# Kernel optimization log

Measured on AMD Instinct MI355X. Metric: run time of the kernel, lower is better.

## Reference

```python
import jax, jax.numpy as jnp
import numpy as np

NUM_HEADS = 12
DROP = 0.5


def setup_inputs() -> dict:
    key = jax.random.key(0)
    k1, k2, k3, k4 = jax.random.split(key, 4)
    B, N, C = 64, 577, 768
    x = jax.random.normal(k1, (B, N, C), dtype=jnp.float32)
    mask = jax.random.uniform(k2, (B, NUM_HEADS, N - 1), dtype=jnp.float32)
    Wqkv = jax.random.normal(k3, (C, 3 * C), dtype=jnp.float32) * 0.02
    bqkv = jnp.zeros((3 * C,), dtype=jnp.float32)
    Wproj = jax.random.normal(k4, (C, C), dtype=jnp.float32) * 0.02
    bproj = jnp.zeros((C,), dtype=jnp.float32)
    return {"x": x, "mask": mask, "Wqkv": Wqkv, "bqkv": bqkv,
            "Wproj": Wproj, "bproj": bproj}


def _drop_tokens(t, idx):
    # t: [B,H,N,D]; keep CLS token, gather sorted random indices from the rest
    rest = jnp.take_along_axis(t[:, :, 1:, :], idx[..., None], axis=2)
    return jnp.concatenate([t[:, :, :1, :], rest], axis=2)


def reference(x, mask, Wqkv, bqkv, Wproj, bproj):
    B, N, C = x.shape
    H = NUM_HEADS
    D = C // H
    scale = D ** -0.5
    target_len = N - int(N * DROP)  # kept tokens incl. CLS

    qkv = (x @ Wqkv + bqkv).reshape(B, N, 3, H, D)
    qkv = jnp.transpose(qkv, (2, 0, 3, 1, 4))  # [3,B,H,N,D]
    q, k, v = qkv[0], qkv[1], qkv[2]

    # random token drop (rand branch): topk of random mask, sort indices
    _, idx = jax.lax.top_k(mask, target_len - 1)  # [B,H,target_len-1]
    idx = jnp.sort(idx, axis=-1)
    k_p = _drop_tokens(k, idx)  # [B,H,target_len,D]
    v_p = _drop_tokens(v, idx)

    attn = jax.nn.softmax(
        jnp.einsum('bhnd,bhmd->bhnm', q, k_p) * scale, axis=-1)
    out = jnp.einsum('bhnm,bhmd->bhnd', attn, v_p)
    out = jnp.transpose(out, (0, 2, 1, 3)).reshape(B, N, C)
    return out @ Wproj + bproj
```

## Files before the change

### kernel.cpp

```cpp
#include <hip/hip_runtime.h>
#include <stdint.h>

#define B_      64
#define N_TOK   577
#define C_      768
#define H_      12
#define BH_     768
#define M_ROWS  36928
#define M_PAD   36992
#define KEEP    289
#define KP      320

typedef __attribute__((ext_vector_type(8))) short   bf16x8;
typedef __attribute__((ext_vector_type(4))) float   floatx4;
typedef __attribute__((ext_vector_type(4))) short   short4v;

static __device__ __forceinline__ unsigned short f2bf(float f) {
  union { float f; unsigned u; } a; a.f = f;
  unsigned u = a.u;
  u = u + 0x7FFFu + ((u >> 16) & 1u);
  return (unsigned short)(u >> 16);
}

static __device__ __forceinline__ void gl_lds16(const void* g, void* l) {
  __builtin_amdgcn_global_load_lds(
      (const __attribute__((address_space(1))) void*)g,
      (__attribute__((address_space(3))) void*)l, 16, 0, 0);
}

__global__ void topk_kernel(const float* __restrict__ mask, int* __restrict__ pos) {
  __shared__ float vals[576];
  __shared__ int woff[9];
  int row = blockIdx.x;
  int t = threadIdx.x;
  float v = mask[(size_t)row * 576 + t];
  vals[t] = v;
  __syncthreads();
  int rank = 0;
  for (int j = 0; j < 576; ++j) {
    float u = vals[j];
    rank += ((u > v) || (u == v && j < t)) ? 1 : 0;
  }
  bool sel = rank < (KEEP - 1);
  unsigned long long ball = __ballot(sel ? 1 : 0);
  int lane = t & 63, w = t >> 6;
  int lp = __popcll(ball & ((1ull << lane) - 1ull));
  if (lane == 0) woff[w] = __popcll(ball);
  __syncthreads();
  int base = 0;
  for (int i = 0; i < w; ++i) base += woff[i];
  pos[(size_t)row * 577 + 1 + t] = sel ? (1 + base + lp) : -1;
  if (t == 0) pos[(size_t)row * 577] = 0;
}

__global__ void convx_kernel(const float* __restrict__ x, unsigned short* __restrict__ xb) {
  size_t i = ((size_t)blockIdx.x * 256 + threadIdx.x) * 4;
  short4v o;
  if (i < (size_t)M_ROWS * C_) {
    float4 v = *(const float4*)(x + i);
    o.x = (short)f2bf(v.x); o.y = (short)f2bf(v.y);
    o.z = (short)f2bf(v.z); o.w = (short)f2bf(v.w);
  } else {
    o.x = 0; o.y = 0; o.z = 0; o.w = 0;
  }
  *(short4v*)(xb + i) = o;
}

__global__ void convwT_kernel(const float* __restrict__ W, unsigned short* __restrict__ Wt,
                              int N) {
  __shared__ unsigned short tile[64 * 72];
  int n0 = blockIdx.x * 64, k0 = blockIdx.y * 64;
  int t = threadIdx.x;
  for (int p = 0; p < 4; ++p) {
    int s = p * 256 + t;
    int k = s >> 4, nc = s & 15;
    float4 v = *(const float4*)(W + (size_t)(k0 + k) * N + n0 + nc * 4);
    short4v o;
    o.x = (short)f2bf(v.x); o.y = (short)f2bf(v.y);
    o.z = (short)f2bf(v.z); o.w = (short)f2bf(v.w);
    *(short4v*)(tile + k * 72 + nc * 4) = o;
  }
  __syncthreads();
  for (int p = 0; p < 2; ++p) {
    int s = p * 256 + t;
    int n = s >> 3, kc = s & 7;
    bf16x8 o;
    for (int j = 0; j < 8; ++j) o[j] = (short)tile[(kc * 8 + j) * 72 + n];
    *(bf16x8*)(Wt + (size_t)(n0 + n) * 768 + k0 + kc * 8) = o;
  }
}

__global__ void zeropad_kernel(unsigned short* __restrict__ Kp, unsigned short* __restrict__ Vp) {
  size_t idx = (size_t)blockIdx.x * 256 + threadIdx.x;
  int bh = (int)(idx / (31 * 64));
  int rem = (int)(idx % (31 * 64));
  int r = KEEP + rem / 64, d = rem & 63;
  size_t o = ((size_t)bh * KP + r) * 64 + d;
  Kp[o] = 0; Vp[o] = 0;
}

static __device__ __forceinline__ void stage_half512(const unsigned short* src,
                                                     unsigned short* lds, int tid) {
#pragma unroll
  for (int c = 0; c < 2; ++c) {
    int s = c * 512 + tid;
    int r = s >> 3, cs = s & 7;
    int gc = (cs ^ (r & 7)) << 3;
    gl_lds16(src + (size_t)r * 768 + gc, lds + s * 8);
  }
}

static __device__ __forceinline__ void gemm256_core(
    const unsigned short* __restrict__ A, const unsigned short* __restrict__ Bt,
    int m0, int n0, int tid, unsigned short* As, unsigned short* Bs,
    floatx4 (&acc)[8][4]) {
  const int lane = tid & 63, wv = tid >> 6;
  const int quad = lane >> 4, lcol = lane & 15;
  const int wm = wv >> 2, wn = wv & 3;
  const int swz = lcol & 7;

#define STG_A(kt, half) stage_half512(A  + (size_t)(m0 + 128*(half)) * 768 + (kt)*64, \
                                      As + ((kt)&1)*16384 + (half)*8192, tid)
#define STG_B(kt, half) stage_half512(Bt + (size_t)(n0 + 128*(half)) * 768 + (kt)*64, \
                                      Bs + ((kt)&1)*16384 + (half)*8192, tid)

  STG_A(0, 0); STG_A(0, 1); STG_B(0, 0); STG_B(0, 1);
  STG_A(1, 0); STG_A(1, 1); STG_B(1, 0);
  asm volatile("s_waitcnt vmcnt(6)" ::: "memory");
  __builtin_amdgcn_s_barrier();

  for (int t = 0; t < 12; ++t) {
    const unsigned short* Asl = As + (t & 1) * 16384;
    const unsigned short* Bsl = Bs + (t & 1) * 16384;

    bf16x8 af[8][2], bfr[4][2];
#pragma unroll
    for (int ks = 0; ks < 2; ++ks) {
      int cc = ks * 4 + quad;
      int co = (cc ^ swz) << 3;
#pragma unroll
      for (int i = 0; i < 8; ++i)
        af[i][ks]  = *(const bf16x8*)(Asl + (wm * 128 + i * 16 + lcol) * 64 + co);
#pragma unroll
      for (int j = 0; j < 4; ++j)
        bfr[j][ks] = *(const bf16x8*)(Bsl + (wn * 64 + j * 16 + lcol) * 64 + co);
    }
    if (t + 1 < 12) STG_B(t + 1, 1);
    asm volatile("s_waitcnt lgkmcnt(0)" ::: "memory");
    __builtin_amdgcn_sched_barrier(0);
    __builtin_amdgcn_s_barrier();
    __builtin_amdgcn_s_setprio(1);
#pragma unroll
    for (int i = 0; i < 2; ++i)
#pragma unroll
      for (int j = 0; j < 4; ++j)
#pragma unroll
        for (int ks = 0; ks < 2; ++ks)
          acc[i][j] = __builtin_amdgcn_mfma_f32_16x16x32_bf16(af[i][ks], bfr[j][ks], acc[i][j], 0, 0, 0);
    __builtin_amdgcn_s_setprio(0);
    __builtin_amdgcn_s_barrier();

#pragma unroll
    for (int p = 1; p < 4; ++p) {
      if (t + 2 < 12) {
        if (p == 1)      STG_A(t + 2, 0);
        else if (p == 2) STG_A(t + 2, 1);
        else             STG_B(t + 2, 0);
      }
      __builtin_amdgcn_s_barrier();
      __builtin_amdgcn_s_setprio(1);
#pragma unroll
      for (int i = 2 * p; i < 2 * p + 2; ++i)
#pragma unroll
        for (int j = 0; j < 4; ++j)
#pragma unroll
          for (int ks = 0; ks < 2; ++ks)
            acc[i][j] = __builtin_amdgcn_mfma_f32_16x16x32_bf16(af[i][ks], bfr[j][ks], acc[i][j], 0, 0, 0);
      __builtin_amdgcn_s_setprio(0);
      if (p == 3) {
        if (t < 10)       asm volatile("s_waitcnt vmcnt(6)" ::: "memory");
        else if (t == 10) asm volatile("s_waitcnt vmcnt(0)" ::: "memory");
      }
      __builtin_amdgcn_s_barrier();
    }
  }
#undef STG_A
#undef STG_B
}

__global__ __launch_bounds__(512) void qkv_gemm_kernel(
    const unsigned short* __restrict__ A, const unsigned short* __restrict__ Bt,
    const float* __restrict__ bias, const int* __restrict__ pos,
    unsigned short* __restrict__ Q, unsigned short* __restrict__ Kp,
    unsigned short* __restrict__ Vp) {
  __shared__ unsigned short As[2 * 16384];
  __shared__ unsigned short Bs[2 * 16384];
  const int tid = threadIdx.x;
  const int lane = tid & 63, wv = tid >> 6;
  const int quad = lane >> 4, lcol = lane & 15;
  const int wm = wv >> 2, wn = wv & 3;
  int orig = blockIdx.x;
  int xcd = orig & 7, loc = orig >> 3;
  int wgid = (xcd < 1 ? xcd * 164 : 164 + (xcd - 1) * 163) + loc;
  const int m_t = wgid / 9, n_t = wgid % 9;
  const int m0 = m_t * 256, n0 = n_t * 256;

  floatx4 acc[8][4] = {};
  gemm256_core(A, Bt, m0, n0, tid, As, Bs, acc);

  const int nbase = n0 + wn * 64;
  const int which = nbase / 768;
  const int h = (nbase - which * 768) >> 6;
  float bv[4];
#pragma unroll
  for (int nt = 0; nt < 4; ++nt) bv[nt] = bias[nbase + nt * 16 + lcol];
#pragma unroll
  for (int i = 0; i < 8; ++i) {
#pragma unroll
    for (int r = 0; r < 4; ++r) {
      int m = m0 + wm * 128 + i * 16 + quad * 4 + r;
      if (m >= M_ROWS) continue;
      int b = m / 577, t = m - b * 577;
      int bh = b * 12 + h;
      if (which == 0) {
        size_t base = ((size_t)bh * 577 + t) * 64;
#pragma unroll
        for (int nt = 0; nt < 4; ++nt)
          Q[base + nt * 16 + lcol] = f2bf(acc[i][nt][r] + bv[nt]);
      } else {
        int p = pos[(size_t)bh * 577 + t];
        if (p >= 0) {
          size_t base = ((size_t)bh * KP + p) * 64;
          if (which == 1) {
            int sw = p & 7;
#pragma unroll
            for (int nt = 0; nt < 4; ++nt) {
              int d = nt * 16 + lcol;
              int d2 = (d & 7) | (((d >> 3) ^ sw) << 3);
              Kp[base + d2] = f2bf(acc[i][nt][r] + bv[nt]);
            }
          } else {
#pragma unroll
            for (int nt = 0; nt < 4; ++nt)
              Vp[base + nt * 16 + lcol] = f2bf(acc[i][nt][r] + bv[nt]);
          }
        }
      }
    }
  }
}

__global__ void transv_kernel(const unsigned short* __restrict__ Vp,
                              unsigned short* __restrict__ VpT) {
  __shared__ unsigned short tile[64 * 72];
  int bh = blockIdx.y, p0 = blockIdx.x * 64;
  int t = threadIdx.x;
  for (int pp = 0; pp < 2; ++pp) {
    int s = pp * 256 + t;
    int p = s >> 3, dc = s & 7;
    bf16x8 v = *(const bf16x8*)(Vp + ((size_t)bh * KP + p0 + p) * 64 + dc * 8);
    *(bf16x8*)(tile + p * 72 + dc * 8) = v;
  }
  __syncthreads();
  for (int pp = 0; pp < 2; ++pp) {
    int s = pp * 256 + t;
    int d = s >> 3, pc = s & 7;
    bf16x8 o;
    for (int j = 0; j < 8; ++j) o[j] = (short)tile[(pc * 8 + j) * 72 + d];
    int pc2 = pc ^ (d & 7);
    *(bf16x8*)(VpT + ((size_t)bh * 64 + d) * KP + p0 + pc2 * 8) = o;
  }
}

__global__ __launch_bounds__(256) void attn_kernel(
    const unsigned short* __restrict__ Q, const unsigned short* __restrict__ Kp,
    const unsigned short* __restrict__ VpT, unsigned short* __restrict__ attnout) {
  __shared__ unsigned short S[320 * 64];
  __shared__ unsigned short Vs[64 * 320];
  const int tid = threadIdx.x;
  const int lane = tid & 63, w = tid >> 6;
  const int quad = lane >> 4, lcol = lane & 15;
  const int g = blockIdx.x;
  const int chunk = g / 80, within = g - chunk * 80;
  const int by = chunk * 8 + (within & 7);
  const int bx = within >> 3;
  const int q0 = bx * 64 + w * 16;

  bf16x8 aq[2];
  {
    int qr = q0 + lcol;
    if (qr < N_TOK) {
      const unsigned short* qp = Q + ((size_t)by * N_TOK + qr) * 64;
      aq[0] = *(const bf16x8*)(qp + quad * 8);
      aq[1] = *(const bf16x8*)(qp + 32 + quad * 8);
    } else {
      bf16x8 z = {0, 0, 0, 0, 0, 0, 0, 0};
      aq[0] = z; aq[1] = z;
    }
  }
  __builtin_amdgcn_sched_barrier(0);

  const unsigned short* kg = Kp + (size_t)by * KP * 64;
#pragma unroll
  for (int c = 0; c < 10; ++c) {
    int s = c * 256 + tid;
    gl_lds16(kg + s * 8, S + s * 8);
  }
  __builtin_amdgcn_sched_barrier(0);
  const unsigned short* vg = VpT + (size_t)by * 64 * KP;
#pragma unroll
  for (int c = 0; c < 10; ++c) {
    int s = c * 256 + tid;
    gl_lds16(vg + s * 8, Vs + s * 8);
  }
  __builtin_amdgcn_sched_barrier(0);

  asm volatile("s_waitcnt vmcnt(10)" ::: "memory");
  __builtin_amdgcn_sched_barrier(0);
  __builtin_amdgcn_s_barrier();

  floatx4 sacc[20] = {};
  __builtin_amdgcn_s_setprio(1);
#pragma unroll
  for (int nt = 0; nt < 19; ++nt) {
    int r16 = nt * 16 + lcol;
    const unsigned short* kb = S + r16 * 64;
    int sw = r16 & 7;
    bf16x8 b0 = *(const bf16x8*)(kb + ((quad ^ sw) << 3));
    bf16x8 b1 = *(const bf16x8*)(kb + (((quad + 4) ^ sw) << 3));
    sacc[nt] = __builtin_amdgcn_mfma_f32_16x16x32_bf16(aq[0], b0, sacc[nt], 0, 0, 0);
    sacc[nt] = __builtin_amdgcn_mfma_f32_16x16x32_bf16(aq[1], b1, sacc[nt], 0, 0, 0);
  }
  __builtin_amdgcn_s_setprio(0);

  const float scale = 0.125f;
  float inva[4];
  for (int r = 0; r < 4; ++r) {
    float mx = -1e30f;
#pragma unroll
    for (int nt = 0; nt < 20; ++nt) {
      int n = nt * 16 + lcol;
      float s = sacc[nt][r] * scale;
      if (n < KEEP) mx = fmaxf(mx, s);
    }
    for (int off = 1; off < 16; off <<= 1) mx = fmaxf(mx, __shfl_xor(mx, off, 64));
    float sum = 0.f;
#pragma unroll
    for (int nt = 0; nt < 20; ++nt) {
      int n = nt * 16 + lcol;
      float e = (n < KEEP) ? __expf(sacc[nt][r] * scale - mx) : 0.f;
      sacc[nt][r] = e;
      sum += e;
    }
    for (int off = 1; off < 16; off <<= 1) sum += __shfl_xor(sum, off, 64);
    inva[r] = 1.f / sum;
  }

  asm volatile("s_waitcnt lgkmcnt(0) vmcnt(0)" ::: "memory");
  __builtin_amdgcn_sched_barrier(0);
  __builtin_amdgcn_s_barrier();

#pragma unroll
  for (int r = 0; r < 4; ++r) {
    int rowl = w * 16 + quad * 4 + r;
    int swp = rowl & 7;
#pragma unroll
    for (int nt = 0; nt < 20; ++nt) {
      int n = nt * 16 + lcol;
      int u = n >> 3;
      int u2 = (u & 0x38) | ((u & 7) ^ swp);
      S[rowl * 320 + u2 * 8 + (n & 7)] = f2bf(sacc[nt][r] * inva[r]);
    }
  }
  asm volatile("s_waitcnt lgkmcnt(0)" ::: "memory");
  __builtin_amdgcn_sched_barrier(0);

  floatx4 oacc[4] = {};
  const int prow = w * 16 + lcol;
  const int psw = prow & 7;
  const int vsw = lcol & 7;
  __builtin_amdgcn_s_setprio(1);
#pragma unroll
  for (int kc = 0; kc < 10; ++kc) {
    int u = kc * 4 + quad;
    int pu2 = (u & 0x38) | ((u & 7) ^ psw);
    bf16x8 pa = *(const bf16x8*)(S + prow * 320 + pu2 * 8);
    int vu2 = (u & 0x38) | ((u & 7) ^ vsw);
#pragma unroll
    for (int nt = 0; nt < 4; ++nt) {
      bf16x8 vb = *(const bf16x8*)(Vs + (nt * 16 + lcol) * 320 + vu2 * 8);
      oacc[nt] = __builtin_amdgcn_mfma_f32_16x16x32_bf16(pa, vb, oacc[nt], 0, 0, 0);
    }
  }
  __builtin_amdgcn_s_setprio(0);

  int b = by / H_, h = by - b * H_;
#pragma unroll
  for (int nt = 0; nt < 4; ++nt)
#pragma unroll
    for (int r = 0; r < 4; ++r) {
      int qr = bx * 64 + w * 16 + quad * 4 + r;
      if (qr < N_TOK)
        attnout[((size_t)(b * N_TOK + qr)) * C_ + h * 64 + nt * 16 + lcol] = f2bf(oacc[nt][r]);
    }
}

__global__ __launch_bounds__(512) void proj_gemm_kernel(
    const unsigned short* __restrict__ A, const unsigned short* __restrict__ Bt,
    const float* __restrict__ bias, float* __restrict__ out) {
  __shared__ unsigned short As[2 * 16384];
  __shared__ unsigned short Bs[2 * 16384];
  const int tid = threadIdx.x;
  const int lane = tid & 63, wv = tid >> 6;
  const int quad = lane >> 4, lcol = lane & 15;
  const int wm = wv >> 2, wn = wv & 3;
  int orig = blockIdx.x;
  int xcd = orig & 7, loc = orig >> 3;
  int wgid = (xcd < 3 ? xcd * 55 : 165 + (xcd - 3) * 54) + loc;
  const int m_t = wgid / 3, n_t = wgid % 3;
  const int m0 = m_t * 256, n0 = n_t * 256;

  floatx4 acc[8][4] = {};
  gemm256_core(A, Bt, m0, n0, tid, As, Bs, acc);

  const int nbase = n0 + wn * 64;
  float bv[4];
#pragma unroll
  for (int nt = 0; nt < 4; ++nt) bv[nt] = bias[nbase + nt * 16 + lcol];
#pragma unroll
  for (int i = 0; i < 8; ++i)
#pragma unroll
    for (int r = 0; r < 4; ++r) {
      int m = m0 + wm * 128 + i * 16 + quad * 4 + r;
      if (m >= M_ROWS) continue;
#pragma unroll
      for (int nt = 0; nt < 4; ++nt)
        out[(size_t)m * C_ + nbase + nt * 16 + lcol] = acc[i][nt][r] + bv[nt];
    }
}

extern "C" void kernel_launch(void* const* d_in, const int* in_sizes, int n_in,
                              void* d_out, int out_size, void* d_ws, size_t ws_size,
                              hipStream_t stream) {
  const float* x     = (const float*)d_in[0];
  const float* mask  = (const float*)d_in[1];
  const float* Wqkv  = (const float*)d_in[2];
  const float* bqkv  = (const float*)d_in[3];
  const float* Wproj = (const float*)d_in[4];
  const float* bproj = (const float*)d_in[5];
  float* out = (float*)d_out;

  char* ws = (char*)d_ws;
  unsigned short* xb     = (unsigned short*)(ws);
  unsigned short* attno  = xb;
  unsigned short* WqkvT  = (unsigned short*)(ws + 56819712);
  unsigned short* WprojT = (unsigned short*)(ws + 60358656);
  int*            pos    = (int*)(ws + 61538304);
  unsigned short* Qb     = (unsigned short*)(ws + 63310848);
  unsigned short* Kpb    = (unsigned short*)(ws + 120032256);
  unsigned short* Vpb    = (unsigned short*)(ws + 151489536);
  unsigned short* VpTb   = (unsigned short*)(ws + 182946816);

  hipLaunchKernelGGL(topk_kernel,     dim3(768),      dim3(576), 0, stream, mask, pos);
  hipLaunchKernelGGL(convx_kernel,    dim3(27744),    dim3(256), 0, stream, x, xb);
  hipLaunchKernelGGL(convwT_kernel,   dim3(36, 12),   dim3(256), 0, stream, Wqkv, WqkvT, 2304);
  hipLaunchKernelGGL(convwT_kernel,   dim3(12, 12),   dim3(256), 0, stream, Wproj, WprojT, 768);
  hipLaunchKernelGGL(zeropad_kernel,  dim3(5952),     dim3(256), 0, stream, Kpb, Vpb);
  hipLaunchKernelGGL(qkv_gemm_kernel, dim3(1305),     dim3(512), 0, stream, xb, WqkvT, bqkv, pos, Qb, Kpb, Vpb);
  hipLaunchKernelGGL(transv_kernel,   dim3(5, 768),   dim3(256), 0, stream, Vpb, VpTb);
  hipLaunchKernelGGL(attn_kernel,     dim3(7680),     dim3(256), 0, stream, Qb, Kpb, VpTb, attno);
  hipLaunchKernelGGL(proj_gemm_kernel,dim3(435),      dim3(512), 0, stream, attno, WprojT, bproj, out);
}
```

Measured before the change: 601.1 us.

## Restructure QKV GEMM main loop with split A-fragment loads and full-tile prefetch

Reworks the software pipeline of the 256x256 bf16 GEMM core. The A fragments are now read from LDS in two halves interleaved with MFMA groups, and both halves of the next-next B tile are staged together instead of one half early. This is meant to overlap LDS reads with MFMA work and lower register pressure from holding all A fragments at once. The cost is more barriers per iteration and different vmcnt accounting, which could cause stalls or races if the counts are wrong.

New measurement: 617.5 us. +2.7%, slower.

```diff
diff --git a/kernel.cpp b/kernel.cpp
--- a/kernel.cpp
+++ b/kernel.cpp
@@ -123,67 +123,72 @@
                                       As + ((kt)&1)*16384 + (half)*8192, tid)
 #define STG_B(kt, half) stage_half512(Bt + (size_t)(n0 + 128*(half)) * 768 + (kt)*64, \
                                       Bs + ((kt)&1)*16384 + (half)*8192, tid)
+#define MFMA_QUAD(q)                                                              \
+  __builtin_amdgcn_s_setprio(1);                                                  \
+  _Pragma("unroll")                                                               \
+  for (int i = 2*(q); i < 2*(q)+2; ++i)                                           \
+    _Pragma("unroll")                                                             \
+    for (int j = 0; j < 4; ++j)                                                   \
+      _Pragma("unroll")                                                           \
+      for (int ks = 0; ks < 2; ++ks)                                              \
+        acc[i][j] = __builtin_amdgcn_mfma_f32_16x16x32_bf16(af[i][ks], bfr[j][ks],\
+                                                            acc[i][j], 0, 0, 0);  \
+  __builtin_amdgcn_s_setprio(0);
 
   STG_A(0, 0); STG_A(0, 1); STG_B(0, 0); STG_B(0, 1);
-  STG_A(1, 0); STG_A(1, 1); STG_B(1, 0);
-  asm volatile("s_waitcnt vmcnt(6)" ::: "memory");
+  STG_A(1, 0); STG_A(1, 1); STG_B(1, 0); STG_B(1, 1);
+  asm volatile("s_waitcnt vmcnt(8)" ::: "memory");
   __builtin_amdgcn_s_barrier();
 
   for (int t = 0; t < 12; ++t) {
     const unsigned short* Asl = As + (t & 1) * 16384;
     const unsigned short* Bsl = Bs + (t & 1) * 16384;
-
     bf16x8 af[8][2], bfr[4][2];
+
 #pragma unroll
     for (int ks = 0; ks < 2; ++ks) {
-      int cc = ks * 4 + quad;
-      int co = (cc ^ swz) << 3;
-#pragma unroll
-      for (int i = 0; i < 8; ++i)
-        af[i][ks]  = *(const bf16x8*)(Asl + (wm * 128 + i * 16 + lcol) * 64 + co);
+      int co = ((ks * 4 + quad) ^ swz) << 3;
 #pragma unroll
       for (int j = 0; j < 4; ++j)
         bfr[j][ks] = *(const bf16x8*)(Bsl + (wn * 64 + j * 16 + lcol) * 64 + co);
-    }
-    if (t + 1 < 12) STG_B(t + 1, 1);
+#pragma unroll
+      for (int i = 0; i < 4; ++i)
+        af[i][ks]  = *(const bf16x8*)(Asl + (wm * 128 + i * 16 + lcol) * 64 + co);
+    }
+    asm volatile("s_waitcnt lgkmcnt(8)" ::: "memory");
+    __builtin_amdgcn_sched_barrier(0);
+    __builtin_amdgcn_s_barrier();
     asm volatile("s_waitcnt lgkmcnt(0)" ::: "memory");
     __builtin_amdgcn_sched_barrier(0);
-    __builtin_amdgcn_s_barrier();
-    __builtin_amdgcn_s_setprio(1);
-#pragma unroll
-    for (int i = 0; i < 2; ++i)
-#pragma unroll
-      for (int j = 0; j < 4; ++j)
-#pragma unroll
-        for (int ks = 0; ks < 2; ++ks)
-          acc[i][j] = __builtin_amdgcn_mfma_f32_16x16x32_bf16(af[i][ks], bfr[j][ks], acc[i][j], 0, 0, 0);
-    __builtin_amdgcn_s_setprio(0);
-    __builtin_amdgcn_s_barrier();
-
-#pragma unroll
-    for (int p = 1; p < 4; ++p) {
-      if (t + 2 < 12) {
-        if (p == 1)      STG_A(t + 2, 0);
-        else if (p == 2) STG_A(t + 2, 1);
-        else             STG_B(t + 2, 0);
-      }
-      __builtin_amdgcn_s_barrier();
-      __builtin_amdgcn_s_setprio(1);
-#pragma unroll
-      for (int i = 2 * p; i < 2 * p + 2; ++i)
-#pragma unroll
-        for (int j = 0; j < 4; ++j)
-#pragma unroll
-          for (int ks = 0; ks < 2; ++ks)
-            acc[i][j] = __builtin_amdgcn_mfma_f32_16x16x32_bf16(af[i][ks], bfr[j][ks], acc[i][j], 0, 0, 0);
-      __builtin_amdgcn_s_setprio(0);
-      if (p == 3) {
-        if (t < 10)       asm volatile("s_waitcnt vmcnt(6)" ::: "memory");
-        else if (t == 10) asm volatile("s_waitcnt vmcnt(0)" ::: "memory");
-      }
-      __builtin_amdgcn_s_barrier();
-    }
-  }
+    MFMA_QUAD(0)
+    __builtin_amdgcn_s_barrier();
+
+#pragma unroll
+    for (int ks = 0; ks < 2; ++ks) {
+      int co = ((ks * 4 + quad) ^ swz) << 3;
+#pragma unroll
+      for (int i = 4; i < 8; ++i)
+        af[i][ks]  = *(const bf16x8*)(Asl + (wm * 128 + i * 16 + lcol) * 64 + co);
+    }
+    __builtin_amdgcn_s_barrier();
+    asm volatile("s_waitcnt lgkmcnt(0)" ::: "memory");
+    __builtin_amdgcn_sched_barrier(0);
+    MFMA_QUAD(1)
+    __builtin_amdgcn_s_barrier();
+
+    if (t + 2 < 12) { STG_A(t + 2, 0); STG_A(t + 2, 1); }
+    __builtin_amdgcn_s_barrier();
+    MFMA_QUAD(2)
+    __builtin_amdgcn_s_barrier();
+
+    if (t + 2 < 12) { STG_B(t + 2, 0); STG_B(t + 2, 1); }
+    __builtin_amdgcn_s_barrier();
+    MFMA_QUAD(3)
+    if (t < 10)       asm volatile("s_waitcnt vmcnt(8)" ::: "memory");
+    else if (t == 10) asm volatile("s_waitcnt vmcnt(0)" ::: "memory");
+    __builtin_amdgcn_s_barrier();
+  }
+#undef MFMA_QUAD
 #undef STG_A
 #undef STG_B
 }
```
